# Optimization experiments

Hardware: AMD Instinct MI355X
Metric: run time of the kernel (lower is better)

Reference implementation:

```python
import jax, jax.numpy as jnp
import numpy as np
import math

B, N, CS, CZ, H, HD, PQ, PV = 1, 512, 1024, 128, 12, 16, 4, 8
INF, EPS = 1e5, 1e-8


def _quat_to_rot(q):
    q = q / jnp.linalg.norm(q, axis=-1, keepdims=True)
    w, x, y, z = q[..., 0], q[..., 1], q[..., 2], q[..., 3]
    R = jnp.stack([
        1 - 2 * (y * y + z * z), 2 * (x * y - w * z), 2 * (x * z + w * y),
        2 * (x * y + w * z), 1 - 2 * (x * x + z * z), 2 * (y * z - w * x),
        2 * (x * z - w * y), 2 * (y * z + w * x), 1 - 2 * (x * x + y * y)
    ], axis=-1)
    return R.reshape(q.shape[:-1] + (3, 3))


def _split3(x):
    # torch.split into 3 chunks along last dim, then stack on new last dim
    d = x.shape[-1] // 3
    return jnp.stack((x[..., :d], x[..., d:2 * d], x[..., 2 * d:]), axis=-1)


def setup_inputs():
    key = jax.random.key(0)
    ks = jax.random.split(key, 12)

    def lin(k, din, dout):
        kw, kb = jax.random.split(k)
        W = jax.random.normal(kw, (din, dout), jnp.float32) / np.float32(np.sqrt(din))
        b = jax.random.normal(kb, (dout,), jnp.float32) * 0.01
        return W, b

    s = jax.random.normal(ks[0], (B, N, CS), jnp.float32)
    z = jax.random.normal(ks[1], (B, N, N, CZ), jnp.float32)
    rot = _quat_to_rot(jax.random.normal(ks[2], (B, N, 4), jnp.float32))
    trans = jax.random.normal(ks[3], (B, N, 3), jnp.float32) * 10.0
    mask = jnp.ones((B, N), jnp.float32)

    Wq, bq = lin(ks[4], CS, H * HD)
    Wkv, bkv = lin(ks[5], CS, 2 * H * HD)
    Wqp, bqp = lin(ks[6], CS, H * PQ * 3)
    Wkvp, bkvp = lin(ks[7], CS, H * (PQ + PV) * 3)
    Wb, bb = lin(ks[8], CZ, H)
    head_w = jax.random.normal(ks[9], (H,), jnp.float32) * 0.5
    Wout, bout = lin(ks[10], H * (CZ + HD + PV * 4), CS)

    return dict(s=s, z=z, rot=rot, trans=trans, mask=mask,
                Wq=Wq, bq=bq, Wkv=Wkv, bkv=bkv, Wqp=Wqp, bqp=bqp,
                Wkvp=Wkvp, bkvp=bkvp, Wb=Wb, bb=bb, head_w=head_w,
                Wout=Wout, bout=bout)


def _ipa(s, z, rot, trans, mask, Wq, bq, Wkv, bkv, Wqp, bqp, Wkvp, bkvp, Wb, bb, head_w, Wout, bout):
    # scalar q, k, v : [B, N, H, HD]
    q = (s @ Wq + bq).reshape(B, N, H, HD)
    kv = (s @ Wkv + bkv).reshape(B, N, H, 2 * HD)
    k, v = kv[..., :HD], kv[..., HD:]

    # point q/k/v in global frame: p' = R p + t
    q_pts = _split3(s @ Wqp + bqp)                      # [B, N, H*PQ, 3]
    q_pts = jnp.einsum('bnij,bnpj->bnpi', rot, q_pts) + trans[:, :, None, :]
    q_pts = q_pts.reshape(B, N, H, PQ, 3)

    kv_pts = _split3(s @ Wkvp + bkvp)                   # [B, N, H*(PQ+PV), 3]
    kv_pts = jnp.einsum('bnij,bnpj->bnpi', rot, kv_pts) + trans[:, :, None, :]
    kv_pts = kv_pts.reshape(B, N, H, PQ + PV, 3)
    k_pts, v_pts = kv_pts[..., :PQ, :], kv_pts[..., PQ:, :]

    # pair bias [B, N, N, H]
    b = z @ Wb + bb

    # scalar attention logits [B, H, N, N]
    a = jnp.einsum('bihd,bjhd->bhij', q, k) * np.float32(math.sqrt(1.0 / (3 * HD)))
    a = a + np.float32(math.sqrt(1.0 / 3)) * jnp.transpose(b, (0, 3, 1, 2))

    # point-distance attention: [B, N, N, H, PQ]
    diff = q_pts[:, :, None] - k_pts[:, None]           # [B, N, N, H, PQ, 3]
    pt_att = jnp.sum(diff * diff, axis=-1)
    hw = jax.nn.softplus(head_w) * np.float32(math.sqrt(1.0 / (3 * (PQ * 9.0 / 2))))
    pt_att = jnp.sum(pt_att * hw[:, None], axis=-1) * (-0.5)   # [B, N, N, H]
    a = a + jnp.transpose(pt_att, (0, 3, 1, 2))

    square_mask = INF * (mask[:, :, None] * mask[:, None, :] - 1.0)  # [B, N, N]
    a = jax.nn.softmax(a + square_mask[:, None], axis=-1)            # [B, H, N, N]

    # scalar output [B, N, H*HD]
    o = jnp.einsum('bhij,bjhd->bihd', a, v).reshape(B, N, H * HD)

    # point output, back to local frame: R^T (p - t)
    o_pt = jnp.einsum('bhij,bjhpc->bihpc', a, v_pts)                 # [B, N, H, PV, 3]
    o_pt = jnp.einsum('bnji,bnhpj->bnhpi', rot, o_pt - trans[:, :, None, None, :])
    o_pt_norm = jnp.sqrt(jnp.sum(o_pt * o_pt, axis=-1) + EPS).reshape(B, N, H * PV)
    o_pt_r = o_pt.reshape(B, N, H * PV, 3)

    # pair output [B, N, H*CZ]
    o_pair = jnp.einsum('bhij,bijc->bihc', a, z).reshape(B, N, H * CZ)

    cat = jnp.concatenate(
        (o, o_pt_r[..., 0], o_pt_r[..., 1], o_pt_r[..., 2], o_pt_norm, o_pair), axis=-1)
    return cat @ Wout + bout


def reference(s, z, rot, trans, mask, Wq, bq, Wkv, bkv, Wqp, bqp, Wkvp, bkvp, Wb, bb, head_w, Wout, bout):
    return _ipa(s, z, rot, trans, mask, Wq, bq, Wkv, bkv, Wqp, bqp, Wkvp, bkvp, Wb, bb, head_w, Wout, bout)
```

## Files before the change

kernel.cpp:

```cpp
#include <hip/hip_runtime.h>
#include <hip/hip_bf16.h>

#define N 512
#define CS 1024
#define CZ 128
#define H 12
#define HD 16
#define KC 2112

__device__ int sniff_f32(const unsigned short* p) {
    int bad = 0;
    for (int i = 0; i < 32; ++i) {
        unsigned short u = p[i];
        int e = (u >> 7) & 0xFF;
        if (e == 0xFF || e >= 141 || (e <= 27 && (u & 0x7FFFu) != 0)) bad++;
    }
    return bad > 0;
}

__device__ __forceinline__ float ld(const void* p, int i, int f32) {
    return f32 ? ((const float*)p)[i]
               : __bfloat162float(((const __hip_bfloat16*)p)[i]);
}

__device__ __forceinline__ float bfu(unsigned short u) {
    return __bfloat162float(*(const __hip_bfloat16*)&u);
}

typedef __attribute__((ext_vector_type(8))) short bf16x8;
typedef __attribute__((ext_vector_type(4))) float f32x4;
typedef __attribute__((ext_vector_type(8))) unsigned short u16x8;

__device__ __forceinline__ unsigned int split_bf16(float x) {
    __hip_bfloat16 hb = __float2bfloat16(x);
    float hf = __bfloat162float(hb);
    __hip_bfloat16 lb = __float2bfloat16(x - hf);
    unsigned int h = *reinterpret_cast<unsigned short*>(&hb);
    unsigned int l = *reinterpret_cast<unsigned short*>(&lb);
    return h | (l << 16);
}

__device__ __forceinline__ void wcat_resolve(int col,
        const void* Wq, const void* Wkv, const void* Wqp, const void* Wkvp,
        const void*& W, int& cc, int& ldim) {
    if (col < 192)      { W = Wq;   cc = col;       ldim = 192; }
    else if (col < 576) { W = Wkv;  cc = col - 192; ldim = 384; }
    else if (col < 720) { W = Wqp;  cc = col - 576; ldim = 144; }
    else                { W = Wkvp; cc = col - 720; ldim = 432; }
}

__global__ void prep_w(const void* Wq, const void* Wkv, const void* Wqp,
                       const void* Wkvp, const void* Wout, const void* s,
                       unsigned short* WcTh, unsigned short* WcTl,
                       unsigned short* WoTh, unsigned short* WoTl,
                       unsigned short* sH, unsigned short* sL)
{
    __shared__ unsigned short th[32][33], tl[32][33];
    __shared__ int flag;
    int t = threadIdx.x;
    if (t == 0) flag = sniff_f32((const unsigned short*)s);
    __syncthreads();
    int f32 = flag;
    int tx = t & 31, ty = t >> 5;
    int b = blockIdx.x;
    if (b < 1152) {
        int ct = b % 36, kt = b / 36;
        int c0 = ct * 32, k0 = kt * 32;
        #pragma unroll
        for (int r = 0; r < 4; ++r) {
            int k = k0 + ty + 8 * r, c = c0 + tx;
            const void* W; int cc, ldim;
            wcat_resolve(c, Wq, Wkv, Wqp, Wkvp, W, cc, ldim);
            unsigned int pe = split_bf16(ld(W, k * ldim + cc, f32));
            th[ty + 8 * r][tx] = (unsigned short)pe;
            tl[ty + 8 * r][tx] = (unsigned short)(pe >> 16);
        }
        __syncthreads();
        #pragma unroll
        for (int r = 0; r < 4; ++r) {
            int c = c0 + ty + 8 * r, k = k0 + tx;
            WcTh[c * CS + k] = th[tx][ty + 8 * r];
            WcTl[c * CS + k] = tl[tx][ty + 8 * r];
        }
    } else if (b < 3264) {
        int bb = b - 1152;
        int ct = bb & 31, kt = bb >> 5;
        int c0 = ct * 32, k0 = kt * 32;
        #pragma unroll
        for (int r = 0; r < 4; ++r) {
            int k = k0 + ty + 8 * r, c = c0 + tx;
            unsigned int pe = split_bf16(ld(Wout, k * CS + c, f32));
            th[ty + 8 * r][tx] = (unsigned short)pe;
            tl[ty + 8 * r][tx] = (unsigned short)(pe >> 16);
        }
        __syncthreads();
        #pragma unroll
        for (int r = 0; r < 4; ++r) {
            int c = c0 + ty + 8 * r, k = k0 + tx;
            WoTh[c * KC + k] = th[tx][ty + 8 * r];
            WoTl[c * KC + k] = tl[tx][ty + 8 * r];
        }
    } else {
        int bb = b - 3264;
        int rt = bb >> 5, ct = bb & 31;
        #pragma unroll
        for (int r = 0; r < 4; ++r) {
            int row = rt * 32 + ty + 8 * r, col = ct * 32 + tx;
            unsigned int pe = split_bf16(ld(s, row * CS + col, f32));
            sH[row * CS + col] = (unsigned short)pe;
            sL[row * CS + col] = (unsigned short)(pe >> 16);
        }
    }
}

__global__ void proj_gemm(const unsigned short* sH, const unsigned short* sL,
                          const unsigned short* BTh, const unsigned short* BTl,
                          float* rawP)
{
    int t = threadIdx.x;
    int bn = blockIdx.x;
    int bm = blockIdx.y;
    int w  = t >> 6, l = t & 63;
    int lr = l & 15, lq = l >> 4;

    int arow = bm * 16 + lr;
    int bcol = bn * 64 + w * 16 + lr;
    const unsigned short* ah_p = sH + arow * CS;
    const unsigned short* al_p = sL + arow * CS;
    const unsigned short* bh_p = BTh + bcol * CS;
    const unsigned short* bl_p = BTl + bcol * CS;

    f32x4 acc = {0.f, 0.f, 0.f, 0.f};
    #pragma unroll 4
    for (int kt = 0; kt < CS / 32; ++kt) {
        int kk = kt * 32 + lq * 8;
        bf16x8 a_h = *(const bf16x8*)(ah_p + kk);
        bf16x8 a_l = *(const bf16x8*)(al_p + kk);
        bf16x8 b_h = *(const bf16x8*)(bh_p + kk);
        bf16x8 b_l = *(const bf16x8*)(bl_p + kk);
        acc = __builtin_amdgcn_mfma_f32_16x16x32_bf16(a_h, b_h, acc, 0, 0, 0);
        acc = __builtin_amdgcn_mfma_f32_16x16x32_bf16(a_h, b_l, acc, 0, 0, 0);
        acc = __builtin_amdgcn_mfma_f32_16x16x32_bf16(a_l, b_h, acc, 0, 0, 0);
    }

    int row0 = bm * 16 + lq * 4;
    #pragma unroll
    for (int r = 0; r < 4; ++r)
        rawP[(row0 + r) * 1152 + bcol] = acc[r];
}

__global__ void proj_post(const float* rawP,
                          const void* bq, const void* bkv,
                          const void* bqp, const void* bkvp,
                          const void* rot, const void* trans, const void* s,
                          float* q, float* kT, float* v,
                          float* qp, float* kpT, float* vp)
{
    __shared__ float rawL[576];
    __shared__ float R[9], T[3];
    __shared__ int flag;
    int t = threadIdx.x;
    int i = blockIdx.x;
    if (t == 0) flag = sniff_f32((const unsigned short*)s);
    __syncthreads();
    int f32 = flag;

    {
        float val = rawP[i * 1152 + t];
        if (t < 192) q[i * 192 + t] = val + ld(bq, t, f32);
        else {
            int cc = t - 192;
            float vv = val + ld(bkv, cc, f32);
            int h = cc >> 5, t2 = cc & 31;
            if (t2 < 16) kT[(h * 16 + t2) * 512 + i] = vv;
            else         v[i * 192 + h * 16 + (t2 - 16)] = vv;
        }
    }
    rawL[t] = rawP[i * 1152 + 576 + t]
            + (t < 144 ? ld(bqp, t, f32) : ld(bkvp, t - 144, f32));
    if (t < 9) R[t] = ld(rot, i * 9 + t, f32);
    if (t >= 16 && t < 19) T[t - 16] = ld(trans, i * 3 + (t - 16), f32);
    __syncthreads();
    if (t < 192) {
        float x, y, zc;
        if (t < 48) { x = rawL[t];        y = rawL[48 + t];   zc = rawL[96 + t]; }
        else { int pk = t - 48;
               x = rawL[144 + pk]; y = rawL[288 + pk]; zc = rawL[432 + pk]; }
        float rx = R[0]*x + R[1]*y + R[2]*zc + T[0];
        float ry = R[3]*x + R[4]*y + R[5]*zc + T[1];
        float rz = R[6]*x + R[7]*y + R[8]*zc + T[2];
        if (t < 48) {
            int h = t >> 2, pp = t & 3, b = i * 144 + h * 12 + pp * 3;
            qp[b] = rx; qp[b + 1] = ry; qp[b + 2] = rz;
        } else {
            int pk = t - 48, h = pk / 12, idx = pk % 12;
            if (idx < 4) {
                int row = h * 12 + idx * 3;
                kpT[(row + 0) * 512 + i] = rx;
                kpT[(row + 1) * 512 + i] = ry;
                kpT[(row + 2) * 512 + i] = rz;
            } else {
                int b = i * 288 + h * 24 + (idx - 4) * 3;
                vp[b] = rx; vp[b + 1] = ry; vp[b + 2] = rz;
            }
        }
    }
}

__global__ void attn_fused(const float* q, const float* kT, const float* v,
                           const float* qp, const float* kpT, const float* vp,
                           const void* z, const void* Wb, const void* bb,
                           const void* head_w, const void* mask,
                           const void* rot, const void* trans, const void* s,
                           unsigned short* catH, unsigned short* catL)
{
    __shared__ float attL[H * N];
    __shared__ float WbL[CZ * H];
    __shared__ float U[6144];
    __shared__ float qL[192], qpL[144];
    __shared__ float RL[9], TL[3], bbL[H], hwL[H];
    __shared__ float miS;
    __shared__ int flag;
    int t = threadIdx.x;
    int i = blockIdx.x;
    if (t == 0) flag = sniff_f32((const unsigned short*)s);
    __syncthreads();
    int f32 = flag;
    for (int idx = t; idx < CZ * H; idx += 512) WbL[idx] = ld(Wb, idx, f32);
    if (t < 192) qL[t] = q[i * 192 + t];
    else if (t < 336) qpL[t - 192] = qp[i * 144 + (t - 192)];
    else if (t < 345) RL[t - 336] = ld(rot, i * 9 + (t - 336), f32);
    else if (t < 348) TL[t - 345] = ld(trans, i * 3 + (t - 345), f32);
    else if (t < 360) bbL[t - 348] = ld(bb, t - 348, f32);
    else if (t < 372) {
        float x = ld(head_w, t - 360, f32);
        float sp = (x > 20.f) ? x : log1pf(expf(x));
        hwL[t - 360] = sp * 0.13608276348795434f;
    }
    else if (t == 372) miS = ld(mask, i, f32);
    __syncthreads();

    {
        int jl = t >> 4, hs = t & 15;
        float4 pf0, pf1; u16x8 pfu;
        if (f32) {
            const float* zrow = (const float*)z + (size_t)i * N * CZ;
            pf0 = *(const float4*)&zrow[t * 4];
            pf1 = *(const float4*)&zrow[(t + 512) * 4];
        } else {
            const unsigned short* zrow = (const unsigned short*)z + (size_t)i * N * CZ;
            pfu = *(const u16x8*)&zrow[t * 8];
        }
        for (int jt = 0; jt < 16; ++jt) {
            __syncthreads();
            if (f32) {
                int f0 = t * 4, f1 = (t + 512) * 4;
                *(float4*)&U[(f0 >> 7) * 132 + (f0 & 127)] = pf0;
                *(float4*)&U[(f1 >> 7) * 132 + (f1 & 127)] = pf1;
            } else {
                int flat = t * 8; int row = flat >> 7, col = flat & 127;
                float4 lo = {bfu(pfu[0]), bfu(pfu[1]), bfu(pfu[2]), bfu(pfu[3])};
                float4 hi = {bfu(pfu[4]), bfu(pfu[5]), bfu(pfu[6]), bfu(pfu[7])};
                *(float4*)&U[row * 132 + col] = lo;
                *(float4*)&U[row * 132 + col + 4] = hi;
            }
            __syncthreads();
            if (jt < 15) {
                if (f32) {
                    const float* zrow = (const float*)z + ((size_t)i * N + (jt + 1) * 32) * CZ;
                    pf0 = *(const float4*)&zrow[t * 4];
                    pf1 = *(const float4*)&zrow[(t + 512) * 4];
                } else {
                    const unsigned short* zrow =
                        (const unsigned short*)z + ((size_t)i * N + (jt + 1) * 32) * CZ;
                    pfu = *(const u16x8*)&zrow[t * 8];
                }
            }
            if (hs < H) {
                float acc = bbL[hs];
                #pragma unroll 8
                for (int c = 0; c < CZ; ++c)
                    acc += U[jl * 132 + c] * WbL[c * H + hs];
                attL[hs * N + jt * 32 + jl] = acc;
            }
        }
    }
    __syncthreads();

    {
        int j = t;
        float mj = ld(mask, j, f32);
        float mterm = 100000.0f * (miS * mj - 1.0f);
        const float* kTj  = kT + j;
        const float* kpTj = kpT + j;
        float bj[H];
        #pragma unroll
        for (int h = 0; h < H; ++h) bj[h] = attL[h * N + j];
        for (int h = 0; h < H; ++h) {
            float qk = 0.f;
            #pragma unroll
            for (int d = 0; d < 16; ++d)
                qk += qL[h * 16 + d] * kTj[(h * 16 + d) * 512];
            float pt = 0.f;
            #pragma unroll
            for (int p = 0; p < 4; ++p) {
                float dx = qpL[h*12 + p*3 + 0] - kpTj[(h*12 + p*3 + 0) * 512];
                float dy = qpL[h*12 + p*3 + 1] - kpTj[(h*12 + p*3 + 1) * 512];
                float dz = qpL[h*12 + p*3 + 2] - kpTj[(h*12 + p*3 + 2) * 512];
                pt += dx * dx + dy * dy + dz * dz;
            }
            attL[h * N + j] = qk * 0.14433756729740643f
                            + 0.5773502691896258f * bj[h]
                            - 0.5f * hwL[h] * pt + mterm;
        }
    }
    __syncthreads();

    {
        int w = t >> 6, l = t & 63;
        for (int h = w; h < H; h += 8) {
            float av[8];
            #pragma unroll
            for (int kk = 0; kk < 8; ++kk) av[kk] = attL[h * N + kk * 64 + l];
            float m = av[0];
            #pragma unroll
            for (int kk = 1; kk < 8; ++kk) m = fmaxf(m, av[kk]);
            for (int off = 1; off < 64; off <<= 1) m = fmaxf(m, __shfl_xor(m, off));
            float ssum = 0.f;
            #pragma unroll
            for (int kk = 0; kk < 8; ++kk) { av[kk] = __expf(av[kk] - m); ssum += av[kk]; }
            for (int off = 1; off < 64; off <<= 1) ssum += __shfl_xor(ssum, off);
            float inv = 1.0f / ssum;
            #pragma unroll
            for (int kk = 0; kk < 8; ++kk) attL[h * N + kk * 64 + l] = av[kk] * inv;
        }
    }
    __syncthreads();

    if (t < 192) {
        int h = t >> 4, d = t & 15;
        float acc = 0.f;
        for (int j = 0; j < N; ++j) acc += attL[h * N + j] * v[j * 192 + h * 16 + d];
        unsigned int pe = split_bf16(acc);
        catH[i * KC + t] = (unsigned short)pe;
        catL[i * KC + t] = (unsigned short)(pe >> 16);
    } else if (t < 288) {
        int hp = t - 192, h = hp >> 3, p = hp & 7;
        float ax = 0, ay = 0, az = 0;
        for (int j = 0; j < N; ++j) {
            float a_ = attL[h * N + j];
            int b2 = j * 288 + h * 24 + p * 3;
            ax += a_ * vp[b2]; ay += a_ * vp[b2 + 1]; az += a_ * vp[b2 + 2];
        }
        float gx = ax - TL[0], gy = ay - TL[1], gz = az - TL[2];
        float lx = RL[0]*gx + RL[3]*gy + RL[6]*gz;
        float ly = RL[1]*gx + RL[4]*gy + RL[7]*gz;
        float lz = RL[2]*gx + RL[5]*gy + RL[8]*gz;
        float nrm = sqrtf(lx*lx + ly*ly + lz*lz + 1e-8f);
        unsigned int pe;
        pe = split_bf16(lx);
        catH[i * KC + 192 + hp] = (unsigned short)pe;
        catL[i * KC + 192 + hp] = (unsigned short)(pe >> 16);
        pe = split_bf16(ly);
        catH[i * KC + 288 + hp] = (unsigned short)pe;
        catL[i * KC + 288 + hp] = (unsigned short)(pe >> 16);
        pe = split_bf16(lz);
        catH[i * KC + 384 + hp] = (unsigned short)pe;
        catL[i * KC + 384 + hp] = (unsigned short)(pe >> 16);
        pe = split_bf16(nrm);
        catH[i * KC + 480 + hp] = (unsigned short)pe;
        catL[i * KC + 480 + hp] = (unsigned short)(pe >> 16);
    }

    {
        int quarter = t >> 7, c = t & 127;
        float pacc[H];
        #pragma unroll
        for (int h = 0; h < H; ++h) pacc[h] = 0.f;
        int j0 = quarter * 128;
        if (f32) {
            const float* zp = (const float*)z + ((size_t)i * N + j0) * CZ + c;
            for (int j = 0; j < 128; ++j) {
                float zc = zp[j * CZ];
                #pragma unroll
                for (int h = 0; h < H; ++h) pacc[h] += attL[h * N + j0 + j] * zc;
            }
        } else {
            const unsigned short* zp =
                (const unsigned short*)z + ((size_t)i * N + j0) * CZ + c;
            for (int j = 0; j < 128; ++j) {
                float zc = bfu(zp[j * CZ]);
                #pragma unroll
                for (int h = 0; h < H; ++h) pacc[h] += attL[h * N + j0 + j] * zc;
            }
        }
        __syncthreads();
        #pragma unroll
        for (int h = 0; h < H; ++h) U[quarter * (H * CZ) + h * CZ + c] = pacc[h];
    }
    __syncthreads();
    for (int idx = t; idx < H * CZ; idx += 512) {
        float vsum = U[idx] + U[1536 + idx] + U[3072 + idx] + U[4608 + idx];
        unsigned int pe = split_bf16(vsum);
        catH[i * KC + 576 + idx] = (unsigned short)pe;
        catL[i * KC + 576 + idx] = (unsigned short)(pe >> 16);
    }
}

__global__ void final_gemm(const unsigned short* AH, const unsigned short* AL,
                           const unsigned short* BTh, const unsigned short* BTl,
                           const void* bout, void* out, const void* s)
{
    __shared__ int flag;
    int t = threadIdx.x;
    int bn = blockIdx.x;
    int bm = blockIdx.y;
    if (t == 0) flag = sniff_f32((const unsigned short*)s);
    __syncthreads();
    int f32 = flag;

    int w  = t >> 6, l = t & 63;
    int lr = l & 15, lq = l >> 4;

    int arow = bm * 16 + lr;
    int bcol = bn * 64 + w * 16 + lr;
    const unsigned short* ah_p = AH + (size_t)arow * KC;
    const unsigned short* al_p = AL + (size_t)arow * KC;
    const unsigned short* bh_p = BTh + (size_t)bcol * KC;
    const unsigned short* bl_p = BTl + (size_t)bcol * KC;

    f32x4 acc = {0.f, 0.f, 0.f, 0.f};
    #pragma unroll 4
    for (int kt = 0; kt < KC / 32; ++kt) {
        int kk = kt * 32 + lq * 8;
        bf16x8 a_h = *(const bf16x8*)(ah_p + kk);
        bf16x8 a_l = *(const bf16x8*)(al_p + kk);
        bf16x8 b_h = *(const bf16x8*)(bh_p + kk);
        bf16x8 b_l = *(const bf16x8*)(bl_p + kk);
        acc = __builtin_amdgcn_mfma_f32_16x16x32_bf16(a_h, b_h, acc, 0, 0, 0);
        acc = __builtin_amdgcn_mfma_f32_16x16x32_bf16(a_h, b_l, acc, 0, 0, 0);
        acc = __builtin_amdgcn_mfma_f32_16x16x32_bf16(a_l, b_h, acc, 0, 0, 0);
    }

    int row0 = bm * 16 + lq * 4;
    float bv = ld(bout, bcol, f32);
    if (f32) {
        float* o = (float*)out;
        #pragma unroll
        for (int r = 0; r < 4; ++r) o[(row0 + r) * CS + bcol] = acc[r] + bv;
    } else {
        __hip_bfloat16* o = (__hip_bfloat16*)out;
        #pragma unroll
        for (int r = 0; r < 4; ++r)
            o[(row0 + r) * CS + bcol] = __float2bfloat16(acc[r] + bv);
    }
}

extern "C" void kernel_launch(void* const* d_in, const int* in_sizes, int n_in,
                              void* d_out, int out_size, void* d_ws, size_t ws_size,
                              hipStream_t stream)
{
    const void* s      = d_in[0];
    const void* z      = d_in[1];
    const void* rot    = d_in[2];
    const void* trans  = d_in[3];
    const void* mask   = d_in[4];
    const void* Wq     = d_in[5];  const void* bq   = d_in[6];
    const void* Wkv    = d_in[7];  const void* bkv  = d_in[8];
    const void* Wqp    = d_in[9];  const void* bqp  = d_in[10];
    const void* Wkvp   = d_in[11]; const void* bkvp = d_in[12];
    const void* Wb     = d_in[13]; const void* bb   = d_in[14];
    const void* head_w = d_in[15];
    const void* Wout   = d_in[16]; const void* bout = d_in[17];

    float* w    = (float*)d_ws;
    float* q    = w;
    float* kT   = q   + 98304;
    float* v    = kT  + 98304;
    float* qp   = v   + 98304;
    float* kpT  = qp  + 73728;
    float* vp   = kpT + 73728;
    float* rawP = vp  + 147456;
    unsigned short* sH   = (unsigned short*)(rawP + 589824);
    unsigned short* sL   = sH   + 524288;
    unsigned short* catH = sL   + 524288;
    unsigned short* catL = catH + 1081344;
    unsigned short* WcTh = catL + 1081344;
    unsigned short* WcTl = WcTh + 1179648;
    unsigned short* WoTh = WcTl + 1179648;
    unsigned short* WoTl = WoTh + 2162688;
    (void)ws_size; (void)in_sizes; (void)n_in; (void)out_size;

    prep_w    <<<3776, 256, 0, stream>>>(Wq, Wkv, Wqp, Wkvp, Wout, s,
                                         WcTh, WcTl, WoTh, WoTl, sH, sL);
    proj_gemm <<<dim3(18, 32), 256, 0, stream>>>(sH, sL, WcTh, WcTl, rawP);
    proj_post <<<512, 576, 0, stream>>>(rawP, bq, bkv, bqp, bkvp, rot, trans, s,
                                        q, kT, v, qp, kpT, vp);
    attn_fused<<<512, 512, 0, stream>>>(q, kT, v, qp, kpT, vp, z, Wb, bb, head_w, mask,
                                        rot, trans, s, catH, catL);
    final_gemm<<<dim3(16, 32), 256, 0, stream>>>(catH, catL, WoTh, WoTl, bout,
                                                 d_out, s);
}
```

Baseline: 436.1 us.

## Split fused attention kernel into logits/softmax and output kernels

```diff
diff --git a/kernel.cpp b/kernel.cpp
--- a/kernel.cpp
+++ b/kernel.cpp
@@ -207,18 +207,17 @@
     }
 }
 
-__global__ void attn_fused(const float* q, const float* kT, const float* v,
-                           const float* qp, const float* kpT, const float* vp,
-                           const void* z, const void* Wb, const void* bb,
-                           const void* head_w, const void* mask,
-                           const void* rot, const void* trans, const void* s,
-                           unsigned short* catH, unsigned short* catL)
+__global__ void attn_logits(const float* q, const float* kT,
+                            const float* qp, const float* kpT,
+                            const void* z, const void* Wb, const void* bb,
+                            const void* head_w, const void* mask, const void* s,
+                            float* attW)
 {
     __shared__ float attL[H * N];
     __shared__ float WbL[CZ * H];
-    __shared__ float U[6144];
+    __shared__ float U[32 * 132];
     __shared__ float qL[192], qpL[144];
-    __shared__ float RL[9], TL[3], bbL[H], hwL[H];
+    __shared__ float bbL[H], hwL[H];
     __shared__ float miS;
     __shared__ int flag;
     int t = threadIdx.x;
@@ -229,10 +228,8 @@
     for (int idx = t; idx < CZ * H; idx += 512) WbL[idx] = ld(Wb, idx, f32);
     if (t < 192) qL[t] = q[i * 192 + t];
     else if (t < 336) qpL[t - 192] = qp[i * 144 + (t - 192)];
-    else if (t < 345) RL[t - 336] = ld(rot, i * 9 + (t - 336), f32);
-    else if (t < 348) TL[t - 345] = ld(trans, i * 3 + (t - 345), f32);
-    else if (t < 360) bbL[t - 348] = ld(bb, t - 348, f32);
-    else if (t < 372) {
+    else if (t >= 348 && t < 360) bbL[t - 348] = ld(bb, t - 348, f32);
+    else if (t >= 360 && t < 372) {
         float x = ld(head_w, t - 360, f32);
         float sp = (x > 20.f) ? x : log1pf(expf(x));
         hwL[t - 360] = sp * 0.13608276348795434f;
@@ -334,6 +331,32 @@
             #pragma unroll
             for (int kk = 0; kk < 8; ++kk) attL[h * N + kk * 64 + l] = av[kk] * inv;
         }
+    }
+    __syncthreads();
+
+    for (int idx = t; idx < H * N; idx += 512)
+        attW[(size_t)i * (H * N) + idx] = attL[idx];
+}
+
+__global__ void attn_out(const float* attW, const float* v, const float* vp,
+                         const void* z, const void* rot, const void* trans,
+                         const void* s, unsigned short* catH, unsigned short* catL)
+{
+    __shared__ float attL[H * N];
+    __shared__ float U[6144];
+    __shared__ float RL[9], TL[3];
+    __shared__ int flag;
+    int t = threadIdx.x;
+    int i = blockIdx.x;
+    if (t == 0) flag = sniff_f32((const unsigned short*)s);
+    __syncthreads();
+    int f32 = flag;
+    for (int idx = t; idx < H * N; idx += 512)
+        attL[idx] = attW[(size_t)i * (H * N) + idx];
+    if (t >= 512 - 16) {
+        int r = t - (512 - 16);
+        if (r < 9) RL[r] = ld(rot, i * 9 + r, f32);
+        else if (r >= 12 && r < 15) TL[r - 12] = ld(trans, i * 3 + (r - 12), f32);
     }
     __syncthreads();
 
@@ -489,15 +512,17 @@
     unsigned short* WcTl = WcTh + 1179648;
     unsigned short* WoTh = WcTl + 1179648;
     unsigned short* WoTl = WoTh + 2162688;
+    float* attW = (float*)(WoTl + 2162688);
     (void)ws_size; (void)in_sizes; (void)n_in; (void)out_size;
 
-    prep_w    <<<3776, 256, 0, stream>>>(Wq, Wkv, Wqp, Wkvp, Wout, s,
-                                         WcTh, WcTl, WoTh, WoTl, sH, sL);
-    proj_gemm <<<dim3(18, 32), 256, 0, stream>>>(sH, sL, WcTh, WcTl, rawP);
-    proj_post <<<512, 576, 0, stream>>>(rawP, bq, bkv, bqp, bkvp, rot, trans, s,
-                                        q, kT, v, qp, kpT, vp);
-    attn_fused<<<512, 512, 0, stream>>>(q, kT, v, qp, kpT, vp, z, Wb, bb, head_w, mask,
-                                        rot, trans, s, catH, catL);
-    final_gemm<<<dim3(16, 32), 256, 0, stream>>>(catH, catL, WoTh, WoTl, bout,
-                                                 d_out, s);
-}
+    prep_w     <<<3776, 256, 0, stream>>>(Wq, Wkv, Wqp, Wkvp, Wout, s,
+                                          WcTh, WcTl, WoTh, WoTl, sH, sL);
+    proj_gemm  <<<dim3(18, 32), 256, 0, stream>>>(sH, sL, WcTh, WcTl, rawP);
+    proj_post  <<<512, 576, 0, stream>>>(rawP, bq, bkv, bqp, bkvp, rot, trans, s,
+                                         q, kT, v, qp, kpT, vp);
+    attn_logits<<<512, 512, 0, stream>>>(q, kT, qp, kpT, z, Wb, bb, head_w, mask,
+                                         s, attW);
+    attn_out   <<<512, 512, 0, stream>>>(attW, v, vp, z, rot, trans, s, catH, catL);
+    final_gemm <<<dim3(16, 32), 256, 0, stream>>>(catH, catL, WoTh, WoTl, bout,
+                                                  d_out, s);
+}
```

Result: slower. 445.6 us (+2.2%).
